# Kernel optimization log

Measured on AMD Instinct MI355X. Metric: run time of the kernel, lower is better.

## Reference

```python
import jax, jax.numpy as jnp
import numpy as np

BS, L, D, H, DC = 8, 8192, 128, 128, 128
C_CONST = 8.0  # rg-lru temperature constant


def _ln(x):
    # LayerNorm without scale/bias (use_bias=False, use_scale=False)
    m = jnp.mean(x, axis=-1, keepdims=True)
    v = jnp.mean(jnp.square(x - m), axis=-1, keepdims=True)
    return (x - m) * jax.lax.rsqrt(v + 1e-6)


def _affine(c, w, b):
    # Dense(features=1)(c)[:, :, None] -> (bs, 1, 1) broadcast scalar per sequence
    return (c @ w + b)[:, :, None]


def _combine(e1, e2):
    a1, b1 = e1
    a2, b2 = e2
    return (a1 * a2, a2 * b1 + b2)


def _linear_scan(a, b, reverse):
    # h_t = a_t * h_{t-1} + b_t (or h_{t+1} when reverse) along seq axis 1
    _, h = jax.lax.associative_scan(_combine, (a, b), axis=1, reverse=reverse)
    return h


def _forward(x, c, cln1_sw, cln1_sb, cln1_bw, cln1_bb, gate1_w, gate1_b,
             rnn_in_w, rnn_in_b, pos_emb, rnn_wi, rnn_bi, rnn_wr, rnn_br, rnn_a,
             rnn_out_w, rnn_out_b, cln2_sw, cln2_sb, cln2_bw, cln2_bb,
             gate2_w, gate2_b, mlp_w1, mlp_b1, mlp_w2, mlp_b2):
    # --- branch 1: conditioned LN -> bidirectional RG-LRU -> gated residual ---
    h = (1.0 + _affine(c, cln1_sw, cln1_sb)) * _ln(x) + _affine(c, cln1_bw, cln1_bb)
    u = _ln(h) @ rnn_in_w + rnn_in_b + pos_emb[None]          # (bs, L, H)
    gi = jax.nn.sigmoid(u @ rnn_wi + rnn_bi)                   # input gate
    gr = jax.nn.sigmoid(u @ rnn_wr + rnn_br)                   # recurrence gate
    at = jnp.exp(C_CONST * gr * jnp.log(rnn_a))                # a_t = a^(c*r_t)
    bt = jnp.sqrt(1.0 - jnp.square(at)) * (gi * u)
    hf = _linear_scan(at, bt, reverse=False)
    hb = _linear_scan(at, bt, reverse=True)
    r = jnp.concatenate([hf, hb], axis=-1) @ rnn_out_w + rnn_out_b  # (bs, L, D)
    x = x + _affine(c, gate1_w, gate1_b) * r
    # --- branch 2: conditioned LN -> gelu MLP -> gated residual ---
    h = (1.0 + _affine(c, cln2_sw, cln2_sb)) * _ln(x) + _affine(c, cln2_bw, cln2_bb)
    m = jax.nn.gelu(h @ mlp_w1 + mlp_b1) @ mlp_w2 + mlp_b2
    return x + _affine(c, gate2_w, gate2_b) * m


def setup_inputs() -> dict:
    key = jax.random.key(0)
    ks = jax.random.split(key, 30)
    def n(k, shape, s=0.05):
        return (jax.random.normal(k, shape) * s).astype(jnp.float32)
    rnn_a = (0.9 + 0.09 * jax.random.uniform(ks[0], (H,))).astype(jnp.float32)
    return {
        "x": jax.random.normal(ks[1], (BS, L, D), jnp.float32),
        "c": jax.random.normal(ks[2], (BS, DC), jnp.float32),
        "cln1_sw": n(ks[3], (DC, 1)), "cln1_sb": n(ks[4], (1,)),
        "cln1_bw": n(ks[5], (DC, 1)), "cln1_bb": n(ks[6], (1,)),
        "gate1_w": n(ks[7], (DC, 1)), "gate1_b": n(ks[8], (1,)),
        "rnn_in_w": n(ks[9], (D, H), 0.1), "rnn_in_b": n(ks[10], (H,)),
        "pos_emb": n(ks[11], (L, H), 0.02),
        "rnn_wi": n(ks[12], (H, H), 0.1), "rnn_bi": n(ks[13], (H,)),
        "rnn_wr": n(ks[14], (H, H), 0.1), "rnn_br": n(ks[15], (H,)),
        "rnn_a": rnn_a,
        "rnn_out_w": n(ks[16], (2 * H, D), 0.1), "rnn_out_b": n(ks[17], (D,)),
        "cln2_sw": n(ks[18], (DC, 1)), "cln2_sb": n(ks[19], (1,)),
        "cln2_bw": n(ks[20], (DC, 1)), "cln2_bb": n(ks[21], (1,)),
        "gate2_w": n(ks[22], (DC, 1)), "gate2_b": n(ks[23], (1,)),
        "mlp_w1": n(ks[24], (D, 4 * D), 0.1), "mlp_b1": n(ks[25], (4 * D,)),
        "mlp_w2": n(ks[26], (4 * D, D), 0.1), "mlp_b2": n(ks[27], (D,)),
    }


def reference(x, c, cln1_sw, cln1_sb, cln1_bw, cln1_bb, gate1_w, gate1_b,
              rnn_in_w, rnn_in_b, pos_emb, rnn_wi, rnn_bi, rnn_wr, rnn_br, rnn_a,
              rnn_out_w, rnn_out_b, cln2_sw, cln2_sb, cln2_bw, cln2_bb,
              gate2_w, gate2_b, mlp_w1, mlp_b1, mlp_w2, mlp_b2):
    return _forward(x, c, cln1_sw, cln1_sb, cln1_bw, cln1_bb, gate1_w, gate1_b,
                    rnn_in_w, rnn_in_b, pos_emb, rnn_wi, rnn_bi, rnn_wr, rnn_br, rnn_a,
                    rnn_out_w, rnn_out_b, cln2_sw, cln2_sb, cln2_bw, cln2_bb,
                    gate2_w, gate2_b, mlp_w1, mlp_b1, mlp_w2, mlp_b2)
```

## Files before the change

### kernel.cpp

```cpp
#include <hip/hip_runtime.h>
#include <hip/hip_bf16.h>

#define BSZ 8
#define SEQ 8192
#define DIM 128
#define NCH 128
#define CLEN 64

typedef unsigned short u16;
typedef unsigned int u32;
typedef short bf16x8 __attribute__((ext_vector_type(8)));
typedef float f32x4  __attribute__((ext_vector_type(4)));

__device__ __forceinline__ float us2f(u16 w){ union{u32 i;float f;}u; u.i=((u32)w)<<16; return u.f; }
__device__ __forceinline__ u16 f2us(float f){
  __hip_bfloat16 h = __float2bfloat16(f);
  union{ __hip_bfloat16 b; u16 s; }u; u.b=h; return u.s;
}
__device__ __forceinline__ float wred64(float v){
  #pragma unroll
  for (int o=1;o<64;o<<=1) v += __shfl_xor(v,o,64);
  return v;
}
__device__ __forceinline__ float red16(float v){
  v += __shfl_xor(v,1,64); v += __shfl_xor(v,2,64);
  v += __shfl_xor(v,4,64); v += __shfl_xor(v,8,64);
  return v;
}
__device__ __forceinline__ float sigmoidf_(float z){ return 1.f/(1.f+__expf(-z)); }
__device__ __forceinline__ float gelu_tanh(float x){
  float y = 0.7978845608028654f * fmaf(0.044715f*x, x*x, x);
  float e = __expf(2.f*y);
  float th = 1.f - 2.f/(e+1.f);
  return 0.5f*x*(1.f+th);
}

__global__ __launch_bounds__(64) void k_aff(
    const float* __restrict__ c,
    const float* w0,const float* w1,const float* w2,const float* w3,const float* w4,const float* w5,
    const float* s0,const float* s1,const float* s2,const float* s3,const float* s4,const float* s5,
    float* __restrict__ aff)
{
  const float* ws[6]={w0,w1,w2,w3,w4,w5};
  const float* bs[6]={s0,s1,s2,s3,s4,s5};
  int l = threadIdx.x;
  for (int b=0;b<BSZ;++b){
    #pragma unroll
    for (int h=0;h<6;++h){
      float v = c[b*128+l]*ws[h][l] + c[b*128+64+l]*ws[h][64+l];
      v = wred64(v);
      if (l==0) aff[b*6+h] = v + bs[h][0];
    }
  }
}

__global__ __launch_bounds__(256) void k_prep(
    const float* __restrict__ w1, const float* __restrict__ w2, const float* __restrict__ wo,
    const float* __restrict__ win, const float* __restrict__ wi, const float* __restrict__ wr,
    u16* __restrict__ w1t, u16* __restrict__ w2t, u16* __restrict__ wot,
    u16* __restrict__ wint, u16* __restrict__ wit, u16* __restrict__ wrt)
{
  int i = blockIdx.x*256 + threadIdx.x;
  { int n=i>>7, k=i&127; w1t[i] = f2us(w1[k*512+n]); }
  { int n=i>>9, k=i&511; w2t[i] = f2us(w2[k*128+n]); }
  if (i < 32768){ int n=i>>8, k=i&255; wot[i] = f2us(wo[k*128+n]); }
  if (i < 16384){
    int n=i>>7, k=i&127;
    wint[i] = f2us(win[k*128+n]);
    wit[i]  = f2us(wi[k*128+n]);
    wrt[i]  = f2us(wr[k*128+n]);
  }
}

__global__ __launch_bounds__(256,2) void k_pre(
    const float* __restrict__ xg, const u16* __restrict__ wint, const float* __restrict__ b_in,
    const float* __restrict__ pos, const u16* __restrict__ wit, const float* __restrict__ b_i,
    const u16* __restrict__ wrt, const float* __restrict__ b_r, const float* __restrict__ avec,
    const float* __restrict__ aff,
    u16* __restrict__ atg, u16* __restrict__ btg,
    float* __restrict__ Ag, float* __restrict__ Bfg, float* __restrict__ Bbg)
{
  __shared__ u16 A_l[CLEN*136];
  __shared__ u16 wT[128*72];
  __shared__ u32 abp[CLEN*DIM];
  const int t  = threadIdx.x;
  const int b  = blockIdx.x >> 7;
  const int ck = blockIdx.x & (NCH-1);
  const size_t base = ((size_t)(b*SEQ + ck*CLEN))*DIM;
  const int lane=t&63, wv=t>>6, col=lane&15, quad=lane>>4;
  const int m0 = wv*16;

  {
    const float s1p = 1.f + aff[b*6+0];
    const int ln = t&63;
    for (int i=0;i<16;++i){
      int r = wv*16 + i;
      float2 v = *(const float2*)(xg + base + (size_t)r*DIM + 2*ln);
      float m  = wred64(v.x+v.y)*(1.f/128.f);
      float d0=v.x-m, d1=v.y-m;
      float var = wred64(d0*d0+d1*d1)*(1.f/128.f);
      float rs = rsqrtf(var + 1e-6f);
      float vz = var*rs*rs;
      float tt2 = s1p*rsqrtf(fmaf(s1p*s1p, vz, 1e-6f));
      float sc = rs*tt2;
      u32 pk = (u32)f2us(d0*sc) | ((u32)f2us(d1*sc)<<16);
      *(u32*)&A_l[r*136 + 2*ln] = pk;
    }
  }

  f32x4 uacc[8];
  #pragma unroll
  for (int n=0;n<8;++n) uacc[n]=(f32x4){0.f,0.f,0.f,0.f};
  for (int c=0;c<2;++c){
    __syncthreads();
    for (int i=t;i<1024;i+=256){
      int n=i>>3, cc=(i&7)*8;
      *(uint4*)&wT[n*72+cc] = *(const uint4*)&wint[(size_t)n*128 + c*64 + cc];
    }
    __syncthreads();
    #pragma unroll
    for (int k2=0;k2<2;++k2){
      bf16x8 av = *(const bf16x8*)&A_l[(m0+col)*136 + c*64 + k2*32 + quad*8];
      #pragma unroll
      for (int n=0;n<8;++n){
        bf16x8 bv = *(const bf16x8*)&wT[(n*16+col)*72 + k2*32 + quad*8];
        uacc[n] = __builtin_amdgcn_mfma_f32_16x16x32_bf16(av, bv, uacc[n], 0,0,0);
      }
    }
  }
  float u_c[8][4];
  #pragma unroll
  for (int n=0;n<8;++n){
    int nc = n*16 + col;
    float bi = b_in[nc];
    #pragma unroll
    for (int r=0;r<4;++r){
      int row = m0 + quad*4 + r;
      u_c[n][r] = uacc[n][r] + bi + pos[(size_t)(ck*CLEN+row)*DIM + nc];
    }
  }
  __syncthreads();

  #pragma unroll
  for (int n=0;n<8;++n){
    #pragma unroll
    for (int r=0;r<4;++r)
      A_l[(m0+quad*4+r)*136 + n*16+col] = f2us(u_c[n][r]);
  }

  f32x4 gacc[8];
  #pragma unroll
  for (int n=0;n<8;++n) gacc[n]=(f32x4){0.f,0.f,0.f,0.f};
  for (int c=0;c<2;++c){
    __syncthreads();
    for (int i=t;i<1024;i+=256){
      int n=i>>3, cc=(i&7)*8;
      *(uint4*)&wT[n*72+cc] = *(const uint4*)&wit[(size_t)n*128 + c*64 + cc];
    }
    __syncthreads();
    #pragma unroll
    for (int k2=0;k2<2;++k2){
      bf16x8 av = *(const bf16x8*)&A_l[(m0+col)*136 + c*64 + k2*32 + quad*8];
      #pragma unroll
      for (int n=0;n<8;++n){
        bf16x8 bv = *(const bf16x8*)&wT[(n*16+col)*72 + k2*32 + quad*8];
        gacc[n] = __builtin_amdgcn_mfma_f32_16x16x32_bf16(av, bv, gacc[n], 0,0,0);
      }
    }
  }
  float gi_c[8][4];
  #pragma unroll
  for (int n=0;n<8;++n){
    float bi = b_i[n*16+col];
    #pragma unroll
    for (int r=0;r<4;++r) gi_c[n][r] = sigmoidf_(gacc[n][r]+bi);
  }

  f32x4 racc[8];
  #pragma unroll
  for (int n=0;n<8;++n) racc[n]=(f32x4){0.f,0.f,0.f,0.f};
  for (int c=0;c<2;++c){
    __syncthreads();
    for (int i=t;i<1024;i+=256){
      int n=i>>3, cc=(i&7)*8;
      *(uint4*)&wT[n*72+cc] = *(const uint4*)&wrt[(size_t)n*128 + c*64 + cc];
    }
    __syncthreads();
    #pragma unroll
    for (int k2=0;k2<2;++k2){
      bf16x8 av = *(const bf16x8*)&A_l[(m0+col)*136 + c*64 + k2*32 + quad*8];
      #pragma unroll
      for (int n=0;n<8;++n){
        bf16x8 bv = *(const bf16x8*)&wT[(n*16+col)*72 + k2*32 + quad*8];
        racc[n] = __builtin_amdgcn_mfma_f32_16x16x32_bf16(av, bv, racc[n], 0,0,0);
      }
    }
  }

  #pragma unroll
  for (int n=0;n<8;++n){
    int nc = n*16 + col;
    float la = __logf(avec[nc]);
    float br = b_r[nc];
    #pragma unroll
    for (int r=0;r<4;++r){
      int row = m0 + quad*4 + r;
      float g = sigmoidf_(racc[n][r]+br);
      float a = __expf(8.f*g*la);
      float bb = sqrtf(fmaxf(1.f-a*a,0.f))*gi_c[n][r]*u_c[n][r];
      u16 ab_ = f2us(a), bb_ = f2us(bb);
      abp[row*DIM+nc] = (u32)ab_ | ((u32)bb_<<16);
      atg[base + (size_t)row*DIM + nc] = ab_;
      btg[base + (size_t)row*DIM + nc] = bb_;
    }
  }
  __syncthreads();

  const int sbase = (b*NCH+ck)*DIM;
  if (t < 128){
    float h=0.f, p=1.f;
    #pragma unroll 4
    for (int tt=0;tt<CLEN;++tt){
      u32 v=abp[tt*DIM+t];
      float a=us2f((u16)v), bb=us2f((u16)(v>>16));
      h=fmaf(a,h,bb); p*=a;
    }
    Ag[sbase+t]=p; Bfg[sbase+t]=h;
  } else {
    int ch=t-128; float h=0.f;
    #pragma unroll 4
    for (int tt=CLEN-1;tt>=0;--tt){
      u32 v=abp[tt*DIM+ch];
      h=fmaf(us2f((u16)v),h,us2f((u16)(v>>16)));
    }
    Bbg[sbase+ch]=h;
  }
}

__global__ __launch_bounds__(128) void k_chunkscan(
    const float* __restrict__ Ag, const float* __restrict__ Bfg, const float* __restrict__ Bbg,
    float* __restrict__ Hf, float* __restrict__ Hb)
{
  const int dir = blockIdx.x >> 3, b = blockIdx.x & 7, ch = threadIdx.x;
  float s = 0.f;
  if (dir==0){
    for (int c=0;c<NCH;++c){ size_t i=((size_t)(b*NCH+c))*DIM+ch; Hf[i]=s; s=fmaf(Ag[i],s,Bfg[i]); }
  } else {
    for (int c=NCH-1;c>=0;--c){ size_t i=((size_t)(b*NCH+c))*DIM+ch; Hb[i]=s; s=fmaf(Ag[i],s,Bbg[i]); }
  }
}

__global__ __launch_bounds__(256,2) void k_scan(
    const u16* __restrict__ atg, const u16* __restrict__ btg,
    const float* __restrict__ Hf, const float* __restrict__ Hb,
    const float* __restrict__ xg, const u16* __restrict__ wot, const float* __restrict__ b_out,
    const float* __restrict__ aff, float* __restrict__ outg)
{
  __shared__ u16 sm[CLEN*DIM*2];
  __shared__ u16 hcat[CLEN*264];
  u16* a_l = sm;
  u16* b_l = sm + CLEN*DIM;
  const int t  = threadIdx.x;
  const int b  = blockIdx.x >> 7;
  const int ck = blockIdx.x & (NCH-1);
  const size_t base = ((size_t)(b*SEQ + ck*CLEN))*DIM;

  {
    const uint4* sa=(const uint4*)(atg+base); const uint4* sb=(const uint4*)(btg+base);
    for (int i=t;i<1024;i+=256){ ((uint4*)a_l)[i]=sa[i]; ((uint4*)b_l)[i]=sb[i]; }
  }
  __syncthreads();

  const int pbase=(b*NCH+ck)*DIM;
  if (t<128){
    float h=Hf[pbase+t];
    #pragma unroll 4
    for (int tt=0;tt<CLEN;++tt){
      h=fmaf(us2f(a_l[tt*DIM+t]),h,us2f(b_l[tt*DIM+t]));
      hcat[tt*264+t]=f2us(h);
    }
  } else {
    int ch=t-128;
    float h=Hb[pbase+ch];
    #pragma unroll 4
    for (int tt=CLEN-1;tt>=0;--tt){
      h=fmaf(us2f(a_l[tt*DIM+ch]),h,us2f(b_l[tt*DIM+ch]));
      hcat[tt*264+128+ch]=f2us(h);
    }
  }
  __syncthreads();

  const int lane=t&63, wv=t>>6, col=lane&15, quad=lane>>4;
  const int m0 = wv*16;
  u16* wol = sm;
  f32x4 acc[8];
  #pragma unroll
  for (int n=0;n<8;++n) acc[n]=(f32x4){0.f,0.f,0.f,0.f};
  for (int chk=0; chk<4; ++chk){
    for (int i=t;i<1024;i+=256){
      int n=i>>3, c=(i&7)*8;
      *(uint4*)&wol[n*72 + c] = *(const uint4*)&wot[(size_t)n*256 + chk*64 + c];
    }
    __syncthreads();
    #pragma unroll
    for (int k2=0;k2<2;++k2){
      bf16x8 av = *(const bf16x8*)&hcat[(m0+col)*264 + chk*64 + k2*32 + quad*8];
      #pragma unroll
      for (int n=0;n<8;++n){
        bf16x8 bv = *(const bf16x8*)&wol[(n*16+col)*72 + k2*32 + quad*8];
        acc[n] = __builtin_amdgcn_mfma_f32_16x16x32_bf16(av, bv, acc[n], 0,0,0);
      }
    }
    __syncthreads();
  }
  const float g1=aff[b*6+2];
  #pragma unroll
  for (int n=0;n<8;++n){
    int nc = n*16 + col;
    float bo = b_out[nc];
    #pragma unroll
    for (int r=0;r<4;++r){
      int row = m0 + quad*4 + r;
      size_t gi = base + (size_t)row*DIM + nc;
      outg[gi] = fmaf(g1, acc[n][r]+bo, xg[gi]);
    }
  }
}

__global__ __launch_bounds__(256,3) void k_mlp(
    const u16* __restrict__ w1t, const float* __restrict__ b1v,
    const u16* __restrict__ w2t, const float* __restrict__ b2v,
    const float* __restrict__ aff, float* __restrict__ outg)
{
  __shared__ u16 h2l[CLEN*136];
  __shared__ u16 wbuf[128*72];
  __shared__ u16 m1p[CLEN*136];
  const int t=threadIdx.x;
  const int b=blockIdx.x>>7;
  const size_t base=(size_t)blockIdx.x*CLEN*DIM;
  const int lane=t&63, wv=t>>6, col=lane&15, quad=lane>>4;
  const int m0 = wv*16;
  const float s2p=1.f+aff[b*6+3], b2a=aff[b*6+4], g2=aff[b*6+5];

  {
    const int cg=t&15, rg=t>>4, j0=cg*8, r0=rg*4;
    #pragma unroll
    for (int ii=0;ii<4;++ii){
      int r=r0+ii;
      const float* xo = outg + base + (size_t)r*DIM + j0;
      float4 a = *(const float4*)xo;
      float4 bq = *(const float4*)(xo+4);
      float o[8]={a.x,a.y,a.z,a.w,bq.x,bq.y,bq.z,bq.w};
      float s=0.f;
      #pragma unroll
      for (int j=0;j<8;++j) s+=o[j];
      s=red16(s); float m=s*(1.f/128.f);
      float q2=0.f;
      #pragma unroll
      for (int j=0;j<8;++j){ float d=o[j]-m; q2+=d*d; }
      q2=red16(q2); float rs=rsqrtf(q2*(1.f/128.f)+1e-6f);
      u32 pk[4];
      #pragma unroll
      for (int q=0;q<4;++q){
        float a0=fmaf((o[2*q]-m)*rs,   s2p, b2a);
        float a1=fmaf((o[2*q+1]-m)*rs, s2p, b2a);
        pk[q]= (u32)f2us(a0) | ((u32)f2us(a1)<<16);
      }
      *(uint4*)&h2l[r*136+j0] = make_uint4(pk[0],pk[1],pk[2],pk[3]);
    }
  }

  f32x4 acc2[8];
  #pragma unroll
  for (int n=0;n<8;++n) acc2[n]=(f32x4){0.f,0.f,0.f,0.f};

  for (int p=0;p<4;++p){
    f32x4 accp[8];
    #pragma unroll
    for (int n=0;n<8;++n) accp[n]=(f32x4){0.f,0.f,0.f,0.f};
    for (int c=0;c<2;++c){
      __syncthreads();
      for (int i=t;i<1024;i+=256){
        int n=i>>3, cc=(i&7)*8;
        *(uint4*)&wbuf[n*72+cc] = *(const uint4*)&w1t[(size_t)(p*128+n)*128 + c*64 + cc];
      }
      __syncthreads();
      #pragma unroll
      for (int k2=0;k2<2;++k2){
        bf16x8 av = *(const bf16x8*)&h2l[(m0+col)*136 + c*64 + k2*32 + quad*8];
        #pragma unroll
        for (int n=0;n<8;++n){
          bf16x8 bv = *(const bf16x8*)&wbuf[(n*16+col)*72 + k2*32 + quad*8];
          accp[n] = __builtin_amdgcn_mfma_f32_16x16x32_bf16(av, bv, accp[n], 0,0,0);
        }
      }
    }
    #pragma unroll
    for (int n=0;n<8;++n){
      int nc = n*16 + col;
      float bb = b1v[p*128 + nc];
      #pragma unroll
      for (int r=0;r<4;++r)
        m1p[(m0+quad*4+r)*136 + nc] = f2us(gelu_tanh(accp[n][r] + bb));
    }
    for (int c=0;c<2;++c){
      __syncthreads();
      for (int i=t;i<1024;i+=256){
        int n=i>>3, cc=(i&7)*8;
        *(uint4*)&wbuf[n*72+cc] = *(const uint4*)&w2t[(size_t)n*512 + p*128 + c*64 + cc];
      }
      __syncthreads();
      #pragma unroll
      for (int k2=0;k2<2;++k2){
        bf16x8 av = *(const bf16x8*)&m1p[(m0+col)*136 + c*64 + k2*32 + quad*8];
        #pragma unroll
        for (int n=0;n<8;++n){
          bf16x8 bv = *(const bf16x8*)&wbuf[(n*16+col)*72 + k2*32 + quad*8];
          acc2[n] = __builtin_amdgcn_mfma_f32_16x16x32_bf16(av, bv, acc2[n], 0,0,0);
        }
      }
    }
  }
  #pragma unroll
  for (int n=0;n<8;++n){
    int nc = n*16 + col;
    float bb = b2v[nc];
    #pragma unroll
    for (int r=0;r<4;++r){
      int row = m0 + quad*4 + r;
      size_t gi = base + (size_t)row*DIM + nc;
      outg[gi] = fmaf(g2, acc2[n][r] + bb, outg[gi]);
    }
  }
}

extern "C" void kernel_launch(void* const* d_in, const int* in_sizes, int n_in,
                              void* d_out, int out_size, void* d_ws, size_t ws_size,
                              hipStream_t stream)
{
  (void)in_sizes; (void)n_in; (void)out_size; (void)ws_size;
  const float* x   =(const float*)d_in[0];
  const float* c   =(const float*)d_in[1];
  const float* c1sw=(const float*)d_in[2];  const float* c1sb=(const float*)d_in[3];
  const float* c1bw=(const float*)d_in[4];  const float* c1bb=(const float*)d_in[5];
  const float* g1w =(const float*)d_in[6];  const float* g1b =(const float*)d_in[7];
  const float* win =(const float*)d_in[8];  const float* binv=(const float*)d_in[9];
  const float* pos =(const float*)d_in[10];
  const float* wi  =(const float*)d_in[11]; const float* biv =(const float*)d_in[12];
  const float* wr  =(const float*)d_in[13]; const float* brv =(const float*)d_in[14];
  const float* av  =(const float*)d_in[15];
  const float* wout=(const float*)d_in[16]; const float* bout=(const float*)d_in[17];
  const float* c2sw=(const float*)d_in[18]; const float* c2sb=(const float*)d_in[19];
  const float* c2bw=(const float*)d_in[20]; const float* c2bb=(const float*)d_in[21];
  const float* g2w =(const float*)d_in[22]; const float* g2b =(const float*)d_in[23];
  const float* w1  =(const float*)d_in[24]; const float* b1v =(const float*)d_in[25];
  const float* w2  =(const float*)d_in[26]; const float* b2v =(const float*)d_in[27];

  float* wsf  = (float*)d_ws;
  float* Ag   = wsf;
  float* Bfg  = Ag   + 131072;
  float* Bbg  = Bfg  + 131072;
  float* Hf   = Bbg  + 131072;
  float* Hb   = Hf   + 131072;
  float* aff  = Hb   + 131072;
  u16*   w1t  = (u16*)(aff + 64);
  u16*   w2t  = w1t + 65536;
  u16*   wot  = w2t + 65536;
  u16*   wint = wot + 32768;
  u16*   wit  = wint + 16384;
  u16*   wrt  = wit  + 16384;
  u16*   atg  = wrt  + 16384;
  u16*   btg  = atg  + 8388608;

  float* outg = (float*)d_out;

  k_aff<<<dim3(1),dim3(64),0,stream>>>(c, c1sw,c1bw,g1w,c2sw,c2bw,g2w,
                                       c1sb,c1bb,g1b,c2sb,c2bb,g2b, aff);
  k_prep<<<dim3(256),dim3(256),0,stream>>>(w1,w2,wout,win,wi,wr,
                                           w1t,w2t,wot,wint,wit,wrt);
  k_pre<<<dim3(BSZ*NCH),dim3(256),0,stream>>>(x,wint,binv,pos,wit,biv,wrt,brv,av,aff,
                                              atg,btg, Ag,Bfg,Bbg);
  k_chunkscan<<<dim3(16),dim3(128),0,stream>>>(Ag,Bfg,Bbg,Hf,Hb);
  k_scan<<<dim3(BSZ*NCH),dim3(256),0,stream>>>(atg,btg,Hf,Hb,x,wot,bout,aff,outg);
  k_mlp<<<dim3(BSZ*NCH),dim3(256),0,stream>>>(w1t,b1v,w2t,b2v,aff,outg);
}
```

Before: 330.1 us.

## Pre-pack weights in MFMA fragment order and read B operands directly from global

Weights are now pre-packed into per-lane MFMA B-fragment order, so each lane loads its bf16x8 operand straight from global or L2. This removes the LDS weight staging and the many __syncthreads around each K-chunk in k_pre, k_scan and k_mlp, and those barriers become per-wave LDS waitcnt fences. The separate a_t and b_t bf16 arrays are merged into one packed u32 array, and the gi and gr GEMMs are fused into one loop. k_pre's occupancy hint is raised to three blocks per SIMD. The trade-off is more global/L2 traffic for weights, which every block now reads directly, and reliance on a per-wave fence being enough where each wave only touches its own rows.

```diff
diff --git a/kernel.cpp b/kernel.cpp
--- a/kernel.cpp
+++ b/kernel.cpp
@@ -34,6 +34,10 @@
   float th = 1.f - 2.f/(e+1.f);
   return 0.5f*x*(1.f+th);
 }
+__device__ __forceinline__ void lds_fence(){
+  asm volatile("s_waitcnt lgkmcnt(0)" ::: "memory");
+  __builtin_amdgcn_sched_barrier(0);
+}
 
 __global__ __launch_bounds__(64) void k_aff(
     const float* __restrict__ c,
@@ -54,6 +58,21 @@
   }
 }
 
+__device__ __forceinline__ void pack_one(const float* __restrict__ W, int N,
+                                         u16* __restrict__ out, int fi)
+{
+  int lane = fi & 63;
+  int k2   = (fi >> 6) & 1;
+  int cn   = fi >> 7;
+  int NB   = N >> 4;
+  int n    = cn % NB, c = cn / NB;
+  int k0   = c*64 + k2*32 + (lane>>4)*8;
+  int col  = n*16 + (lane&15);
+  u16* o = out + (size_t)fi*8;
+  #pragma unroll
+  for (int j=0;j<8;++j) o[j] = f2us(W[(size_t)(k0+j)*N + col]);
+}
+
 __global__ __launch_bounds__(256) void k_prep(
     const float* __restrict__ w1, const float* __restrict__ w2, const float* __restrict__ wo,
     const float* __restrict__ win, const float* __restrict__ wi, const float* __restrict__ wr,
@@ -61,27 +80,23 @@
     u16* __restrict__ wint, u16* __restrict__ wit, u16* __restrict__ wrt)
 {
   int i = blockIdx.x*256 + threadIdx.x;
-  { int n=i>>7, k=i&127; w1t[i] = f2us(w1[k*512+n]); }
-  { int n=i>>9, k=i&511; w2t[i] = f2us(w2[k*128+n]); }
-  if (i < 32768){ int n=i>>8, k=i&255; wot[i] = f2us(wo[k*128+n]); }
-  if (i < 16384){
-    int n=i>>7, k=i&127;
-    wint[i] = f2us(win[k*128+n]);
-    wit[i]  = f2us(wi[k*128+n]);
-    wrt[i]  = f2us(wr[k*128+n]);
-  }
-}
-
-__global__ __launch_bounds__(256,2) void k_pre(
+  if      (i <  8192) pack_one(w1, 512, w1t, i);
+  else if (i < 16384) pack_one(w2, 128, w2t, i-8192);
+  else if (i < 20480) pack_one(wo, 128, wot, i-16384);
+  else if (i < 22528) pack_one(win,128, wint,i-20480);
+  else if (i < 24576) pack_one(wi, 128, wit, i-22528);
+  else                pack_one(wr, 128, wrt, i-24576);
+}
+
+__global__ __launch_bounds__(256,3) void k_pre(
     const float* __restrict__ xg, const u16* __restrict__ wint, const float* __restrict__ b_in,
     const float* __restrict__ pos, const u16* __restrict__ wit, const float* __restrict__ b_i,
     const u16* __restrict__ wrt, const float* __restrict__ b_r, const float* __restrict__ avec,
     const float* __restrict__ aff,
-    u16* __restrict__ atg, u16* __restrict__ btg,
+    u32* __restrict__ abg,
     float* __restrict__ Ag, float* __restrict__ Bfg, float* __restrict__ Bbg)
 {
   __shared__ u16 A_l[CLEN*136];
-  __shared__ u16 wT[128*72];
   __shared__ u32 abp[CLEN*DIM];
   const int t  = threadIdx.x;
   const int b  = blockIdx.x >> 7;
@@ -107,23 +122,19 @@
       *(u32*)&A_l[r*136 + 2*ln] = pk;
     }
   }
+  lds_fence();
 
   f32x4 uacc[8];
   #pragma unroll
   for (int n=0;n<8;++n) uacc[n]=(f32x4){0.f,0.f,0.f,0.f};
+  #pragma unroll
   for (int c=0;c<2;++c){
-    __syncthreads();
-    for (int i=t;i<1024;i+=256){
-      int n=i>>3, cc=(i&7)*8;
-      *(uint4*)&wT[n*72+cc] = *(const uint4*)&wint[(size_t)n*128 + c*64 + cc];
-    }
-    __syncthreads();
     #pragma unroll
     for (int k2=0;k2<2;++k2){
       bf16x8 av = *(const bf16x8*)&A_l[(m0+col)*136 + c*64 + k2*32 + quad*8];
       #pragma unroll
       for (int n=0;n<8;++n){
-        bf16x8 bv = *(const bf16x8*)&wT[(n*16+col)*72 + k2*32 + quad*8];
+        bf16x8 bv = *(const bf16x8*)&wint[(size_t)(((c*8+n)*2+k2)*64+lane)*8];
         uacc[n] = __builtin_amdgcn_mfma_f32_16x16x32_bf16(av, bv, uacc[n], 0,0,0);
       }
     }
@@ -139,60 +150,28 @@
       u_c[n][r] = uacc[n][r] + bi + pos[(size_t)(ck*CLEN+row)*DIM + nc];
     }
   }
-  __syncthreads();
-
   #pragma unroll
   for (int n=0;n<8;++n){
     #pragma unroll
     for (int r=0;r<4;++r)
       A_l[(m0+quad*4+r)*136 + n*16+col] = f2us(u_c[n][r]);
   }
-
-  f32x4 gacc[8];
-  #pragma unroll
-  for (int n=0;n<8;++n) gacc[n]=(f32x4){0.f,0.f,0.f,0.f};
+  lds_fence();
+
+  f32x4 gacc[8], racc[8];
+  #pragma unroll
+  for (int n=0;n<8;++n){ gacc[n]=(f32x4){0.f,0.f,0.f,0.f}; racc[n]=(f32x4){0.f,0.f,0.f,0.f}; }
+  #pragma unroll
   for (int c=0;c<2;++c){
-    __syncthreads();
-    for (int i=t;i<1024;i+=256){
-      int n=i>>3, cc=(i&7)*8;
-      *(uint4*)&wT[n*72+cc] = *(const uint4*)&wit[(size_t)n*128 + c*64 + cc];
-    }
-    __syncthreads();
     #pragma unroll
     for (int k2=0;k2<2;++k2){
       bf16x8 av = *(const bf16x8*)&A_l[(m0+col)*136 + c*64 + k2*32 + quad*8];
       #pragma unroll
       for (int n=0;n<8;++n){
-        bf16x8 bv = *(const bf16x8*)&wT[(n*16+col)*72 + k2*32 + quad*8];
-        gacc[n] = __builtin_amdgcn_mfma_f32_16x16x32_bf16(av, bv, gacc[n], 0,0,0);
-      }
-    }
-  }
-  float gi_c[8][4];
-  #pragma unroll
-  for (int n=0;n<8;++n){
-    float bi = b_i[n*16+col];
-    #pragma unroll
-    for (int r=0;r<4;++r) gi_c[n][r] = sigmoidf_(gacc[n][r]+bi);
-  }
-
-  f32x4 racc[8];
-  #pragma unroll
-  for (int n=0;n<8;++n) racc[n]=(f32x4){0.f,0.f,0.f,0.f};
-  for (int c=0;c<2;++c){
-    __syncthreads();
-    for (int i=t;i<1024;i+=256){
-      int n=i>>3, cc=(i&7)*8;
-      *(uint4*)&wT[n*72+cc] = *(const uint4*)&wrt[(size_t)n*128 + c*64 + cc];
-    }
-    __syncthreads();
-    #pragma unroll
-    for (int k2=0;k2<2;++k2){
-      bf16x8 av = *(const bf16x8*)&A_l[(m0+col)*136 + c*64 + k2*32 + quad*8];
-      #pragma unroll
-      for (int n=0;n<8;++n){
-        bf16x8 bv = *(const bf16x8*)&wT[(n*16+col)*72 + k2*32 + quad*8];
-        racc[n] = __builtin_amdgcn_mfma_f32_16x16x32_bf16(av, bv, racc[n], 0,0,0);
+        bf16x8 bgi = *(const bf16x8*)&wit[(size_t)(((c*8+n)*2+k2)*64+lane)*8];
+        gacc[n] = __builtin_amdgcn_mfma_f32_16x16x32_bf16(av, bgi, gacc[n], 0,0,0);
+        bf16x8 bgr = *(const bf16x8*)&wrt[(size_t)(((c*8+n)*2+k2)*64+lane)*8];
+        racc[n] = __builtin_amdgcn_mfma_f32_16x16x32_bf16(av, bgr, racc[n], 0,0,0);
       }
     }
   }
@@ -202,16 +181,17 @@
     int nc = n*16 + col;
     float la = __logf(avec[nc]);
     float br = b_r[nc];
+    float bi = b_i[nc];
     #pragma unroll
     for (int r=0;r<4;++r){
       int row = m0 + quad*4 + r;
-      float g = sigmoidf_(racc[n][r]+br);
-      float a = __expf(8.f*g*la);
-      float bb = sqrtf(fmaxf(1.f-a*a,0.f))*gi_c[n][r]*u_c[n][r];
-      u16 ab_ = f2us(a), bb_ = f2us(bb);
-      abp[row*DIM+nc] = (u32)ab_ | ((u32)bb_<<16);
-      atg[base + (size_t)row*DIM + nc] = ab_;
-      btg[base + (size_t)row*DIM + nc] = bb_;
+      float gi = sigmoidf_(gacc[n][r]+bi);
+      float g  = sigmoidf_(racc[n][r]+br);
+      float a  = __expf(8.f*g*la);
+      float bb = sqrtf(fmaxf(1.f-a*a,0.f))*gi*u_c[n][r];
+      u32 pk = (u32)f2us(a) | ((u32)f2us(bb)<<16);
+      abp[row*DIM+nc] = pk;
+      abg[base + (size_t)row*DIM + nc] = pk;
     }
   }
   __syncthreads();
@@ -251,23 +231,21 @@
 }
 
 __global__ __launch_bounds__(256,2) void k_scan(
-    const u16* __restrict__ atg, const u16* __restrict__ btg,
+    const u32* __restrict__ abg,
     const float* __restrict__ Hf, const float* __restrict__ Hb,
     const float* __restrict__ xg, const u16* __restrict__ wot, const float* __restrict__ b_out,
     const float* __restrict__ aff, float* __restrict__ outg)
 {
-  __shared__ u16 sm[CLEN*DIM*2];
+  __shared__ u32 ab_l[CLEN*DIM];
   __shared__ u16 hcat[CLEN*264];
-  u16* a_l = sm;
-  u16* b_l = sm + CLEN*DIM;
   const int t  = threadIdx.x;
   const int b  = blockIdx.x >> 7;
   const int ck = blockIdx.x & (NCH-1);
   const size_t base = ((size_t)(b*SEQ + ck*CLEN))*DIM;
 
   {
-    const uint4* sa=(const uint4*)(atg+base); const uint4* sb=(const uint4*)(btg+base);
-    for (int i=t;i<1024;i+=256){ ((uint4*)a_l)[i]=sa[i]; ((uint4*)b_l)[i]=sb[i]; }
+    const uint4* src=(const uint4*)(abg+base);
+    for (int i=t;i<2048;i+=256) ((uint4*)ab_l)[i]=src[i];
   }
   __syncthreads();
 
@@ -276,7 +254,8 @@
     float h=Hf[pbase+t];
     #pragma unroll 4
     for (int tt=0;tt<CLEN;++tt){
-      h=fmaf(us2f(a_l[tt*DIM+t]),h,us2f(b_l[tt*DIM+t]));
+      u32 v=ab_l[tt*DIM+t];
+      h=fmaf(us2f((u16)v),h,us2f((u16)(v>>16)));
       hcat[tt*264+t]=f2us(h);
     }
   } else {
@@ -284,7 +263,8 @@
     float h=Hb[pbase+ch];
     #pragma unroll 4
     for (int tt=CLEN-1;tt>=0;--tt){
-      h=fmaf(us2f(a_l[tt*DIM+ch]),h,us2f(b_l[tt*DIM+ch]));
+      u32 v=ab_l[tt*DIM+ch];
+      h=fmaf(us2f((u16)v),h,us2f((u16)(v>>16)));
       hcat[tt*264+128+ch]=f2us(h);
     }
   }
@@ -292,26 +272,20 @@
 
   const int lane=t&63, wv=t>>6, col=lane&15, quad=lane>>4;
   const int m0 = wv*16;
-  u16* wol = sm;
   f32x4 acc[8];
   #pragma unroll
   for (int n=0;n<8;++n) acc[n]=(f32x4){0.f,0.f,0.f,0.f};
+  #pragma unroll
   for (int chk=0; chk<4; ++chk){
-    for (int i=t;i<1024;i+=256){
-      int n=i>>3, c=(i&7)*8;
-      *(uint4*)&wol[n*72 + c] = *(const uint4*)&wot[(size_t)n*256 + chk*64 + c];
-    }
-    __syncthreads();
     #pragma unroll
     for (int k2=0;k2<2;++k2){
       bf16x8 av = *(const bf16x8*)&hcat[(m0+col)*264 + chk*64 + k2*32 + quad*8];
       #pragma unroll
       for (int n=0;n<8;++n){
-        bf16x8 bv = *(const bf16x8*)&wol[(n*16+col)*72 + k2*32 + quad*8];
+        bf16x8 bv = *(const bf16x8*)&wot[(size_t)(((chk*8+n)*2+k2)*64+lane)*8];
         acc[n] = __builtin_amdgcn_mfma_f32_16x16x32_bf16(av, bv, acc[n], 0,0,0);
       }
     }
-    __syncthreads();
   }
   const float g1=aff[b*6+2];
   #pragma unroll
@@ -333,7 +307,6 @@
     const float* __restrict__ aff, float* __restrict__ outg)
 {
   __shared__ u16 h2l[CLEN*136];
-  __shared__ u16 wbuf[128*72];
   __shared__ u16 m1p[CLEN*136];
   const int t=threadIdx.x;
   const int b=blockIdx.x>>7;
@@ -369,32 +342,30 @@
       *(uint4*)&h2l[r*136+j0] = make_uint4(pk[0],pk[1],pk[2],pk[3]);
     }
   }
+  lds_fence();
 
   f32x4 acc2[8];
   #pragma unroll
   for (int n=0;n<8;++n) acc2[n]=(f32x4){0.f,0.f,0.f,0.f};
 
+  #pragma unroll
   for (int p=0;p<4;++p){
     f32x4 accp[8];
     #pragma unroll
     for (int n=0;n<8;++n) accp[n]=(f32x4){0.f,0.f,0.f,0.f};
+    #pragma unroll
     for (int c=0;c<2;++c){
-      __syncthreads();
-      for (int i=t;i<1024;i+=256){
-        int n=i>>3, cc=(i&7)*8;
-        *(uint4*)&wbuf[n*72+cc] = *(const uint4*)&w1t[(size_t)(p*128+n)*128 + c*64 + cc];
-      }
-      __syncthreads();
       #pragma unroll
       for (int k2=0;k2<2;++k2){
         bf16x8 av = *(const bf16x8*)&h2l[(m0+col)*136 + c*64 + k2*32 + quad*8];
         #pragma unroll
         for (int n=0;n<8;++n){
-          bf16x8 bv = *(const bf16x8*)&wbuf[(n*16+col)*72 + k2*32 + quad*8];
+          bf16x8 bv = *(const bf16x8*)&w1t[(size_t)(((c*32 + p*8+n)*2+k2)*64+lane)*8];
           accp[n] = __builtin_amdgcn_mfma_f32_16x16x32_bf16(av, bv, accp[n], 0,0,0);
         }
       }
     }
+    lds_fence();
     #pragma unroll
     for (int n=0;n<8;++n){
       int nc = n*16 + col;
@@ -403,19 +374,15 @@
       for (int r=0;r<4;++r)
         m1p[(m0+quad*4+r)*136 + nc] = f2us(gelu_tanh(accp[n][r] + bb));
     }
+    lds_fence();
+    #pragma unroll
     for (int c=0;c<2;++c){
-      __syncthreads();
-      for (int i=t;i<1024;i+=256){
-        int n=i>>3, cc=(i&7)*8;
-        *(uint4*)&wbuf[n*72+cc] = *(const uint4*)&w2t[(size_t)n*512 + p*128 + c*64 + cc];
-      }
-      __syncthreads();
       #pragma unroll
       for (int k2=0;k2<2;++k2){
         bf16x8 av = *(const bf16x8*)&m1p[(m0+col)*136 + c*64 + k2*32 + quad*8];
         #pragma unroll
         for (int n=0;n<8;++n){
-          bf16x8 bv = *(const bf16x8*)&wbuf[(n*16+col)*72 + k2*32 + quad*8];
+          bf16x8 bv = *(const bf16x8*)&w2t[(size_t)((((p*2+c)*8+n)*2+k2)*64+lane)*8];
           acc2[n] = __builtin_amdgcn_mfma_f32_16x16x32_bf16(av, bv, acc2[n], 0,0,0);
         }
       }
@@ -469,18 +436,17 @@
   u16*   wint = wot + 32768;
   u16*   wit  = wint + 16384;
   u16*   wrt  = wit  + 16384;
-  u16*   atg  = wrt  + 16384;
-  u16*   btg  = atg  + 8388608;
+  u32*   abg  = (u32*)(wrt + 16384);
 
   float* outg = (float*)d_out;
 
   k_aff<<<dim3(1),dim3(64),0,stream>>>(c, c1sw,c1bw,g1w,c2sw,c2bw,g2w,
                                        c1sb,c1bb,g1b,c2sb,c2bb,g2b, aff);
-  k_prep<<<dim3(256),dim3(256),0,stream>>>(w1,w2,wout,win,wi,wr,
+  k_prep<<<dim3(104),dim3(256),0,stream>>>(w1,w2,wout,win,wi,wr,
                                            w1t,w2t,wot,wint,wit,wrt);
   k_pre<<<dim3(BSZ*NCH),dim3(256),0,stream>>>(x,wint,binv,pos,wit,biv,wrt,brv,av,aff,
-                                              atg,btg, Ag,Bfg,Bbg);
+                                              abg, Ag,Bfg,Bbg);
   k_chunkscan<<<dim3(16),dim3(128),0,stream>>>(Ag,Bfg,Bbg,Hf,Hb);
-  k_scan<<<dim3(BSZ*NCH),dim3(256),0,stream>>>(atg,btg,Hf,Hb,x,wot,bout,aff,outg);
+  k_scan<<<dim3(BSZ*NCH),dim3(256),0,stream>>>(abg,Hf,Hb,x,wot,bout,aff,outg);
   k_mlp<<<dim3(BSZ*NCH),dim3(256),0,stream>>>(w1t,b1v,w2t,b2v,aff,outg);
 }
```

Measured after the change: 352.3 us. +6.7%, slower.
